# Optimization experiments

Measured on AMD Instinct MI355X. Metric: run time of the kernel, lower is better.

Reference implementation:

```python
import jax, jax.numpy as jnp
import numpy as np

N = 100000
E = 800000
D_IN = 512
D_OUT = 512
EPS = 1e-5


def setup_inputs() -> dict:
    key = jax.random.key(0)
    k = jax.random.split(key, 7)
    x = jax.random.normal(k[0], (N, D_IN), dtype=jnp.float32)
    edge_index = jax.random.randint(k[1], (2, E), 0, N, dtype=jnp.int64)
    # PyG SAGEConv params: lin_l (applied to aggregated neighbors, has bias), lin_r (root weight, no bias)
    W_l = jax.random.normal(k[2], (D_OUT, D_IN), dtype=jnp.float32) * 0.02
    b_l = jnp.zeros((D_OUT,), dtype=jnp.float32)
    W_r = jax.random.normal(k[3], (D_OUT, D_IN), dtype=jnp.float32) * 0.02
    # BatchNorm1d affine params (track_running_stats=False -> always batch stats)
    gamma = jnp.ones((D_OUT,), dtype=jnp.float32)
    beta = jnp.zeros((D_OUT,), dtype=jnp.float32)
    return {"x": x, "edge_index": edge_index, "W_l": W_l, "b_l": b_l,
            "W_r": W_r, "gamma": gamma, "beta": beta}


def reference(x, edge_index, W_l, b_l, W_r, gamma, beta):
    n = x.shape[0]
    src, dst = edge_index[0], edge_index[1]
    # mean-aggregate neighbor features: for each dst node, mean of x[src]
    summed = jax.ops.segment_sum(x[src], dst, num_segments=n)          # [N, D_IN]
    cnt = jax.ops.segment_sum(jnp.ones((src.shape[0],), x.dtype), dst, num_segments=n)
    aggr = summed / jnp.maximum(cnt, 1.0)[:, None]                      # zero-degree -> 0
    # SAGEConv: lin_l(aggr) + lin_r(x)
    h = aggr @ W_l.T + b_l + x @ W_r.T                                  # [N, D_OUT]
    # BatchNorm1d with batch statistics (biased variance), then ReLU
    mu = jnp.mean(h, axis=0)
    var = jnp.mean(jnp.square(h - mu), axis=0)
    h_norm = (h - mu) * jax.lax.rsqrt(var + EPS) * gamma + beta
    return jax.nn.relu(h_norm)
```

## Files before the change

kernel.cpp:

```cpp
#include <hip/hip_runtime.h>
#include <stdint.h>

#define D 512
#define K_TOT 1024
#define EPS 1e-5f
#define CHUNK 1024

typedef __bf16 bf16;
typedef bf16 bf16x8 __attribute__((ext_vector_type(8)));
typedef float f32x4 __attribute__((ext_vector_type(4)));

__global__ void k_convert(const float* __restrict__ x, bf16* __restrict__ xb, size_t total8) {
  size_t i = (size_t)blockIdx.x * blockDim.x + threadIdx.x;
  size_t stride = (size_t)gridDim.x * blockDim.x;
  for (; i < total8; i += stride) {
    float4 a = ((const float4*)x)[i * 2];
    float4 b = ((const float4*)x)[i * 2 + 1];
    bf16x8 v = { (bf16)a.x, (bf16)a.y, (bf16)a.z, (bf16)a.w,
                 (bf16)b.x, (bf16)b.y, (bf16)b.z, (bf16)b.w };
    *(bf16x8*)&xb[i * 8] = v;
  }
}

__global__ void k_degree(const int* __restrict__ dst, int* __restrict__ cnt, int E) {
  int i = blockIdx.x * blockDim.x + threadIdx.x;
  int stride = gridDim.x * blockDim.x;
  for (; i < E; i += stride) atomicAdd(&cnt[dst[i]], 1);
}

__global__ void k_blocksum(const int* __restrict__ cnt, int* __restrict__ bsum, int n) {
  __shared__ int red[4];
  int b = blockIdx.x;
  int base = b * CHUNK;
  int s = 0;
  for (int i = threadIdx.x; i < CHUNK; i += 256) {
    int idx = base + i;
    s += (idx < n) ? cnt[idx] : 0;
  }
#pragma unroll
  for (int o = 32; o > 0; o >>= 1) s += __shfl_down(s, o);
  if ((threadIdx.x & 63) == 0) red[threadIdx.x >> 6] = s;
  __syncthreads();
  if (threadIdx.x == 0) bsum[b] = red[0] + red[1] + red[2] + red[3];
}

__global__ void k_scanb(int* __restrict__ bsum, int* __restrict__ bbase, int nb,
                        int* __restrict__ off, int n, int E) {
  if (threadIdx.x == 0) {
    int run = 0;
    for (int i = 0; i < nb; ++i) { bbase[i] = run; run += bsum[i]; }
    off[n] = E;
  }
}

__global__ void k_offsets(const int* __restrict__ cnt, const int* __restrict__ bbase,
                          int* __restrict__ off, int n) {
  __shared__ int tsum[256];
  int b = blockIdx.x;
  int i0 = b * CHUNK + threadIdx.x * 4;
  int vals[4];
  int s = 0;
#pragma unroll
  for (int j = 0; j < 4; ++j) {
    int idx = i0 + j;
    vals[j] = (idx < n) ? cnt[idx] : 0;
    s += vals[j];
  }
  tsum[threadIdx.x] = s;
  __syncthreads();
  for (int d = 1; d < 256; d <<= 1) {
    int v = (threadIdx.x >= d) ? tsum[threadIdx.x - d] : 0;
    __syncthreads();
    tsum[threadIdx.x] += v;
    __syncthreads();
  }
  int excl = tsum[threadIdx.x] - s + bbase[b];
#pragma unroll
  for (int j = 0; j < 4; ++j) {
    int idx = i0 + j;
    if (idx < n) off[idx] = excl;
    excl += vals[j];
  }
}

__global__ void k_fill(const int* __restrict__ src, const int* __restrict__ dst,
                       const int* __restrict__ off, int* __restrict__ cur,
                       int* __restrict__ csr, int E) {
  int i = blockIdx.x * blockDim.x + threadIdx.x;
  int stride = gridDim.x * blockDim.x;
  for (; i < E; i += stride) {
    int d = dst[i];
    int pos = off[d] + atomicAdd(&cur[d], 1);
    csr[pos] = src[i];
  }
}

__device__ __forceinline__ void acc8(float* c, uint4 u) {
  c[0] += __uint_as_float(u.x << 16);
  c[1] += __uint_as_float(u.x & 0xffff0000u);
  c[2] += __uint_as_float(u.y << 16);
  c[3] += __uint_as_float(u.y & 0xffff0000u);
  c[4] += __uint_as_float(u.z << 16);
  c[5] += __uint_as_float(u.z & 0xffff0000u);
  c[6] += __uint_as_float(u.w << 16);
  c[7] += __uint_as_float(u.w & 0xffff0000u);
}

__global__ __launch_bounds__(256) void k_gather(const bf16* __restrict__ xb,
                                                const int* __restrict__ off,
                                                const int* __restrict__ csr,
                                                bf16* __restrict__ aggr, int n) {
  int node = blockIdx.x * 4 + (threadIdx.x >> 6);
  if (node >= n) return;
  int lane = threadIdx.x & 63;
  int s0 = off[node], s1 = off[node + 1];
  float c[8] = {0.f, 0.f, 0.f, 0.f, 0.f, 0.f, 0.f, 0.f};
  int j = s0;
  for (; j + 3 < s1; j += 4) {
    int i0 = csr[j], i1 = csr[j + 1], i2 = csr[j + 2], i3 = csr[j + 3];
    uint4 u0 = *((const uint4*)(xb + (size_t)i0 * D) + lane);
    uint4 u1 = *((const uint4*)(xb + (size_t)i1 * D) + lane);
    uint4 u2 = *((const uint4*)(xb + (size_t)i2 * D) + lane);
    uint4 u3 = *((const uint4*)(xb + (size_t)i3 * D) + lane);
    acc8(c, u0);
    acc8(c, u1);
    acc8(c, u2);
    acc8(c, u3);
  }
  for (; j < s1; ++j) {
    int a = csr[j];
    uint4 u = *((const uint4*)(xb + (size_t)a * D) + lane);
    acc8(c, u);
  }
  float rinv = (s1 > s0) ? 1.0f / (float)(s1 - s0) : 0.0f;
  bf16x8 out = { (bf16)(c[0] * rinv), (bf16)(c[1] * rinv), (bf16)(c[2] * rinv), (bf16)(c[3] * rinv),
                 (bf16)(c[4] * rinv), (bf16)(c[5] * rinv), (bf16)(c[6] * rinv), (bf16)(c[7] * rinv) };
  *(bf16x8*)&aggr[(size_t)node * D + lane * 8] = out;
}

__global__ void k_build_W(const float* __restrict__ Wl, const float* __restrict__ Wr,
                          bf16* __restrict__ Wc) {
  int i = blockIdx.x * blockDim.x + threadIdx.x;
  if (i >= D * K_TOT) return;
  int o = i >> 10, k = i & 1023;
  float v = (k < D) ? Wr[o * D + k] : Wl[o * D + (k - D)];
  Wc[i] = (bf16)v;
}

__device__ __forceinline__ void gl_lds16(const bf16* g, bf16* l) {
  __builtin_amdgcn_global_load_lds((const __attribute__((address_space(1))) unsigned int*)g,
                                   (__attribute__((address_space(3))) unsigned int*)l, 16, 0, 0);
}

__global__ __launch_bounds__(512, 2) void k_gemm(const bf16* __restrict__ Xb,
                                                 const bf16* __restrict__ Aggr,
                                                 const bf16* __restrict__ Wc,
                                                 const float* __restrict__ bias,
                                                 float* __restrict__ C,
                                                 float* __restrict__ stat, int M) {
  __shared__ __align__(16) bf16 sA0[256 * 64];
  __shared__ __align__(16) bf16 sB0[256 * 64];
  __shared__ __align__(16) bf16 sA1[256 * 64];
  __shared__ __align__(16) bf16 sB1[256 * 64];
  const int tid = threadIdx.x;
  const int lane = tid & 63;
  const int wid = tid >> 6;
  const int wm = wid >> 2;
  const int wn = wid & 3;
  const int fr = lane & 15;
  const int fq = lane >> 4;

  const int bx = blockIdx.x >> 1;
  const int by = blockIdx.x & 1;
  const size_t rowA0 = (size_t)bx * 256;
  const int rowB0 = by * 256;

  const int lrow = tid >> 3;
  const int scol = (((tid & 7) ^ (lrow & 7)) * 8);
  const bf16* pA_x = Xb + (rowA0 + lrow) * D + scol;
  const bf16* pA_g = Aggr + (rowA0 + lrow) * D + scol;
  const bf16* pB = Wc + (size_t)(rowB0 + lrow) * K_TOT + scol;
  bf16* ldsA0 = &sA0[lrow * 64 + (tid & 7) * 8];
  bf16* ldsB0 = &sB0[lrow * 64 + (tid & 7) * 8];
  bf16* ldsA1 = &sA1[lrow * 64 + (tid & 7) * 8];
  bf16* ldsB1 = &sB1[lrow * 64 + (tid & 7) * 8];

  f32x4 acc[8][4] = {};

#define STAGE(t, la, lb) do {                                                   \
    const bf16* As = ((t) < 8) ? pA_x : pA_g;                                   \
    const int ko = ((t) & 7) * 64;                                              \
    _Pragma("unroll")                                                           \
    for (int i = 0; i < 4; ++i) {                                               \
      gl_lds16(As + (size_t)i * 64 * D + ko, (la) + i * 64 * 64);               \
      gl_lds16(pB + (size_t)i * 64 * K_TOT + (t) * 64, (lb) + i * 64 * 64);     \
    }                                                                           \
  } while (0)

#define COMPUTE(sa, sb) do {                                                    \
    _Pragma("unroll")                                                           \
    for (int kk = 0; kk < 2; ++kk) {                                            \
      const int cx = ((kk * 4 + fq) ^ (fr & 7)) * 8;                            \
      bf16x8 aF[8], bF[4];                                                      \
      _Pragma("unroll")                                                         \
      for (int m = 0; m < 8; ++m)                                               \
        aF[m] = *(const bf16x8*)&(sa)[(wm * 128 + m * 16 + fr) * 64 + cx];      \
      _Pragma("unroll")                                                         \
      for (int nn = 0; nn < 4; ++nn)                                            \
        bF[nn] = *(const bf16x8*)&(sb)[(wn * 64 + nn * 16 + fr) * 64 + cx];     \
      _Pragma("unroll")                                                         \
      for (int m = 0; m < 8; ++m)                                               \
        _Pragma("unroll")                                                       \
        for (int nn = 0; nn < 4; ++nn)                                          \
          acc[m][nn] = __builtin_amdgcn_mfma_f32_16x16x32_bf16(aF[m], bF[nn], acc[m][nn], 0, 0, 0); \
    }                                                                           \
  } while (0)

  STAGE(0, ldsA0, ldsB0);
  __syncthreads();
#pragma unroll 1
  for (int t = 0; t < 16; t += 2) {
    STAGE(t + 1, ldsA1, ldsB1);
    COMPUTE(sA0, sB0);
    __syncthreads();
    if (t + 2 < 16) STAGE(t + 2, ldsA0, ldsB0);
    COMPUTE(sA1, sB1);
    __syncthreads();
  }
#undef STAGE
#undef COMPUTE

  const int rowb = (int)rowA0 + wm * 128;
  const int colb = rowB0 + wn * 64;
  float s[4] = {0.f, 0.f, 0.f, 0.f}, q[4] = {0.f, 0.f, 0.f, 0.f};
#pragma unroll
  for (int nn = 0; nn < 4; ++nn) {
    int col = colb + nn * 16 + fr;
    float bv = bias[col];
#pragma unroll
    for (int m = 0; m < 8; ++m) {
      int row0 = rowb + m * 16 + fq * 4;
#pragma unroll
      for (int r = 0; r < 4; ++r) {
        int row = row0 + r;
        if (row < M) {
          float v = acc[m][nn][r] + bv;
          C[(size_t)row * D + col] = v;
          s[nn] += v;
          q[nn] += v * v;
        }
      }
    }
  }
#pragma unroll
  for (int nn = 0; nn < 4; ++nn) {
    float sv = s[nn], qv = q[nn];
    sv += __shfl_down(sv, 32); sv += __shfl_down(sv, 16);
    qv += __shfl_down(qv, 32); qv += __shfl_down(qv, 16);
    if (lane < 16) {
      int col = colb + nn * 16 + fr;
      atomicAdd(&stat[col], sv);
      atomicAdd(&stat[D + col], qv);
    }
  }
}

__global__ void k_finalize(const float* __restrict__ stat, const float* __restrict__ gamma,
                           const float* __restrict__ beta, float* __restrict__ ss, float invn) {
  int c = threadIdx.x;
  float mu = stat[c] * invn;
  float var = stat[D + c] * invn - mu * mu;
  float sc = gamma[c] * rsqrtf(var + EPS);
  ss[c] = sc;
  ss[D + c] = beta[c] - mu * sc;
}

__global__ void k_apply(float* __restrict__ h, const float* __restrict__ ss, int n) {
  size_t i = (size_t)blockIdx.x * blockDim.x + threadIdx.x;
  size_t stride = (size_t)gridDim.x * blockDim.x;
  size_t total = (size_t)n * (D / 4);
  for (; i < total; i += stride) {
    int c4 = ((int)i & 127) * 4;
    float4 v = ((const float4*)h)[i];
    float4 sc = *(const float4*)&ss[c4];
    float4 sh = *(const float4*)&ss[D + c4];
    float4 o;
    o.x = fmaxf(v.x * sc.x + sh.x, 0.f);
    o.y = fmaxf(v.y * sc.y + sh.y, 0.f);
    o.z = fmaxf(v.z * sc.z + sh.z, 0.f);
    o.w = fmaxf(v.w * sc.w + sh.w, 0.f);
    ((float4*)h)[i] = o;
  }
}

extern "C" void kernel_launch(void* const* d_in, const int* in_sizes, int n_in,
                              void* d_out, int out_size, void* d_ws, size_t ws_size,
                              hipStream_t stream) {
  const float* x = (const float*)d_in[0];
  const int* ei = (const int*)d_in[1];
  const float* Wl = (const float*)d_in[2];
  const float* bl = (const float*)d_in[3];
  const float* Wr = (const float*)d_in[4];
  const float* gamma = (const float*)d_in[5];
  const float* beta = (const float*)d_in[6];
  float* out = (float*)d_out;

  const int E = in_sizes[1] / 2;
  const int n = in_sizes[0] / D;
  const int Mpad = ((n + 255) / 256) * 256;
  const int nb = (n + CHUNK - 1) / CHUNK;

  char* ws = (char*)d_ws;
  size_t off_b = 0;
  bf16* Xb   = (bf16*)(ws + off_b); off_b += (size_t)Mpad * D * sizeof(bf16);
  bf16* Aggr = (bf16*)(ws + off_b); off_b += (size_t)Mpad * D * sizeof(bf16);
  bf16* Wc   = (bf16*)(ws + off_b); off_b += (size_t)D * K_TOT * sizeof(bf16);
  int* cnt   = (int*)(ws + off_b);  off_b += (size_t)n * sizeof(int);
  int* offs  = (int*)(ws + off_b);  off_b += (size_t)(n + 1) * sizeof(int);
  int* cur   = (int*)(ws + off_b);  off_b += (size_t)n * sizeof(int);
  int* csr   = (int*)(ws + off_b);  off_b += (size_t)E * sizeof(int);
  int* bsum  = (int*)(ws + off_b);  off_b += 512 * sizeof(int);
  int* bbase = (int*)(ws + off_b);  off_b += 512 * sizeof(int);
  float* stat = (float*)(ws + off_b); off_b += 2 * D * sizeof(float);
  float* ss   = (float*)(ws + off_b);

  const int* srcIdx = ei;
  const int* dstIdx = ei + E;

  hipMemsetAsync(cnt, 0, (size_t)n * sizeof(int), stream);
  hipMemsetAsync(cur, 0, (size_t)n * sizeof(int), stream);
  hipMemsetAsync(stat, 0, 2 * D * sizeof(float), stream);
  hipMemsetAsync(Xb + (size_t)n * D, 0, (size_t)(Mpad - n) * D * sizeof(bf16), stream);
  hipMemsetAsync(Aggr + (size_t)n * D, 0, (size_t)(Mpad - n) * D * sizeof(bf16), stream);

  k_convert<<<2048, 256, 0, stream>>>(x, Xb, (size_t)n * D / 8);
  k_degree<<<1024, 256, 0, stream>>>(dstIdx, cnt, E);
  k_blocksum<<<nb, 256, 0, stream>>>(cnt, bsum, n);
  k_scanb<<<1, 64, 0, stream>>>(bsum, bbase, nb, offs, n, E);
  k_offsets<<<nb, 256, 0, stream>>>(cnt, bbase, offs, n);
  k_fill<<<1024, 256, 0, stream>>>(srcIdx, dstIdx, offs, cur, csr, E);
  k_build_W<<<(D * K_TOT + 255) / 256, 256, 0, stream>>>(Wl, Wr, Wc);
  k_gather<<<(n + 3) / 4, 256, 0, stream>>>(Xb, offs, csr, Aggr, n);
  k_gemm<<<(Mpad / 256) * 2, 512, 0, stream>>>(Xb, Aggr, Wc, bl, out, stat, n);
  k_finalize<<<1, 512, 0, stream>>>(stat, gamma, beta, ss, 1.0f / (float)n);
  k_apply<<<2048, 256, 0, stream>>>(out, ss, n);
}
```

Baseline: 579.8 us.

## Shrink GEMM tile to 128x128, swizzle block order, unroll gather by eight

The GEMM tile shrinks from 256x256 with 512 threads to 128x128 with 256 threads, cutting per-block LDS and accumulator registers so more blocks can be resident at once. Block indices are remapped in chunks of eight, apparently so neighbouring blocks share A and B tiles in cache. The neighbour gather adds an 8-way unrolled loop to keep more loads in flight. Smaller tiles lower arithmetic intensity and raise global traffic for re-reading A and W. The swizzle also assumes the grid size is a multiple of eight.

```diff
diff --git a/kernel.cpp b/kernel.cpp
--- a/kernel.cpp
+++ b/kernel.cpp
@@ -116,16 +116,27 @@
   int s0 = off[node], s1 = off[node + 1];
   float c[8] = {0.f, 0.f, 0.f, 0.f, 0.f, 0.f, 0.f, 0.f};
   int j = s0;
+  for (; j + 7 < s1; j += 8) {
+    int i0 = csr[j], i1 = csr[j + 1], i2 = csr[j + 2], i3 = csr[j + 3];
+    int i4 = csr[j + 4], i5 = csr[j + 5], i6 = csr[j + 6], i7 = csr[j + 7];
+    uint4 u0 = *((const uint4*)(xb + (size_t)i0 * D) + lane);
+    uint4 u1 = *((const uint4*)(xb + (size_t)i1 * D) + lane);
+    uint4 u2 = *((const uint4*)(xb + (size_t)i2 * D) + lane);
+    uint4 u3 = *((const uint4*)(xb + (size_t)i3 * D) + lane);
+    uint4 u4 = *((const uint4*)(xb + (size_t)i4 * D) + lane);
+    uint4 u5 = *((const uint4*)(xb + (size_t)i5 * D) + lane);
+    uint4 u6 = *((const uint4*)(xb + (size_t)i6 * D) + lane);
+    uint4 u7 = *((const uint4*)(xb + (size_t)i7 * D) + lane);
+    acc8(c, u0); acc8(c, u1); acc8(c, u2); acc8(c, u3);
+    acc8(c, u4); acc8(c, u5); acc8(c, u6); acc8(c, u7);
+  }
   for (; j + 3 < s1; j += 4) {
     int i0 = csr[j], i1 = csr[j + 1], i2 = csr[j + 2], i3 = csr[j + 3];
     uint4 u0 = *((const uint4*)(xb + (size_t)i0 * D) + lane);
     uint4 u1 = *((const uint4*)(xb + (size_t)i1 * D) + lane);
     uint4 u2 = *((const uint4*)(xb + (size_t)i2 * D) + lane);
     uint4 u3 = *((const uint4*)(xb + (size_t)i3 * D) + lane);
-    acc8(c, u0);
-    acc8(c, u1);
-    acc8(c, u2);
-    acc8(c, u3);
+    acc8(c, u0); acc8(c, u1); acc8(c, u2); acc8(c, u3);
   }
   for (; j < s1; ++j) {
     int a = csr[j];
@@ -152,28 +163,30 @@
                                    (__attribute__((address_space(3))) unsigned int*)l, 16, 0, 0);
 }
 
-__global__ __launch_bounds__(512, 2) void k_gemm(const bf16* __restrict__ Xb,
+__global__ __launch_bounds__(256, 2) void k_gemm(const bf16* __restrict__ Xb,
                                                  const bf16* __restrict__ Aggr,
                                                  const bf16* __restrict__ Wc,
                                                  const float* __restrict__ bias,
                                                  float* __restrict__ C,
                                                  float* __restrict__ stat, int M) {
-  __shared__ __align__(16) bf16 sA0[256 * 64];
-  __shared__ __align__(16) bf16 sB0[256 * 64];
-  __shared__ __align__(16) bf16 sA1[256 * 64];
-  __shared__ __align__(16) bf16 sB1[256 * 64];
+  __shared__ __align__(16) bf16 sA0[128 * 64];
+  __shared__ __align__(16) bf16 sB0[128 * 64];
+  __shared__ __align__(16) bf16 sA1[128 * 64];
+  __shared__ __align__(16) bf16 sB1[128 * 64];
   const int tid = threadIdx.x;
   const int lane = tid & 63;
   const int wid = tid >> 6;
-  const int wm = wid >> 2;
-  const int wn = wid & 3;
+  const int wm = wid >> 1;
+  const int wn = wid & 1;
   const int fr = lane & 15;
   const int fq = lane >> 4;
 
-  const int bx = blockIdx.x >> 1;
-  const int by = blockIdx.x & 1;
-  const size_t rowA0 = (size_t)bx * 256;
-  const int rowB0 = by * 256;
+  const int cpx = gridDim.x >> 3;
+  const int sw = (blockIdx.x & 7) * cpx + (blockIdx.x >> 3);
+  const int bx = sw >> 2;
+  const int by = sw & 3;
+  const size_t rowA0 = (size_t)bx * 128;
+  const int rowB0 = by * 128;
 
   const int lrow = tid >> 3;
   const int scol = (((tid & 7) ^ (lrow & 7)) * 8);
@@ -185,15 +198,15 @@
   bf16* ldsA1 = &sA1[lrow * 64 + (tid & 7) * 8];
   bf16* ldsB1 = &sB1[lrow * 64 + (tid & 7) * 8];
 
-  f32x4 acc[8][4] = {};
+  f32x4 acc[4][4] = {};
 
 #define STAGE(t, la, lb) do {                                                   \
     const bf16* As = ((t) < 8) ? pA_x : pA_g;                                   \
     const int ko = ((t) & 7) * 64;                                              \
     _Pragma("unroll")                                                           \
-    for (int i = 0; i < 4; ++i) {                                               \
-      gl_lds16(As + (size_t)i * 64 * D + ko, (la) + i * 64 * 64);               \
-      gl_lds16(pB + (size_t)i * 64 * K_TOT + (t) * 64, (lb) + i * 64 * 64);     \
+    for (int j = 0; j < 4; ++j) {                                               \
+      gl_lds16(As + (size_t)j * 32 * D + ko, (la) + j * 32 * 64);               \
+      gl_lds16(pB + (size_t)j * 32 * K_TOT + (t) * 64, (lb) + j * 32 * 64);     \
     }                                                                           \
   } while (0)
 
@@ -201,15 +214,15 @@
     _Pragma("unroll")                                                           \
     for (int kk = 0; kk < 2; ++kk) {                                            \
       const int cx = ((kk * 4 + fq) ^ (fr & 7)) * 8;                            \
-      bf16x8 aF[8], bF[4];                                                      \
+      bf16x8 aF[4], bF[4];                                                      \
       _Pragma("unroll")                                                         \
-      for (int m = 0; m < 8; ++m)                                               \
-        aF[m] = *(const bf16x8*)&(sa)[(wm * 128 + m * 16 + fr) * 64 + cx];      \
+      for (int m = 0; m < 4; ++m)                                               \
+        aF[m] = *(const bf16x8*)&(sa)[(wm * 64 + m * 16 + fr) * 64 + cx];       \
       _Pragma("unroll")                                                         \
       for (int nn = 0; nn < 4; ++nn)                                            \
         bF[nn] = *(const bf16x8*)&(sb)[(wn * 64 + nn * 16 + fr) * 64 + cx];     \
       _Pragma("unroll")                                                         \
-      for (int m = 0; m < 8; ++m)                                               \
+      for (int m = 0; m < 4; ++m)                                               \
         _Pragma("unroll")                                                       \
         for (int nn = 0; nn < 4; ++nn)                                          \
           acc[m][nn] = __builtin_amdgcn_mfma_f32_16x16x32_bf16(aF[m], bF[nn], acc[m][nn], 0, 0, 0); \
@@ -230,7 +243,7 @@
 #undef STAGE
 #undef COMPUTE
 
-  const int rowb = (int)rowA0 + wm * 128;
+  const int rowb = (int)rowA0 + wm * 64;
   const int colb = rowB0 + wn * 64;
   float s[4] = {0.f, 0.f, 0.f, 0.f}, q[4] = {0.f, 0.f, 0.f, 0.f};
 #pragma unroll
@@ -238,7 +251,7 @@
     int col = colb + nn * 16 + fr;
     float bv = bias[col];
 #pragma unroll
-    for (int m = 0; m < 8; ++m) {
+    for (int m = 0; m < 4; ++m) {
       int row0 = rowb + m * 16 + fq * 4;
 #pragma unroll
       for (int r = 0; r < 4; ++r) {
@@ -341,7 +354,7 @@
   k_fill<<<1024, 256, 0, stream>>>(srcIdx, dstIdx, offs, cur, csr, E);
   k_build_W<<<(D * K_TOT + 255) / 256, 256, 0, stream>>>(Wl, Wr, Wc);
   k_gather<<<(n + 3) / 4, 256, 0, stream>>>(Xb, offs, csr, Aggr, n);
-  k_gemm<<<(Mpad / 256) * 2, 512, 0, stream>>>(Xb, Aggr, Wc, bl, out, stat, n);
+  k_gemm<<<(Mpad / 128) * 4, 256, 0, stream>>>(Xb, Aggr, Wc, bl, out, stat, n);
   k_finalize<<<1, 512, 0, stream>>>(stat, gamma, beta, ss, 1.0f / (float)n);
   k_apply<<<2048, 256, 0, stream>>>(out, ss, n);
 }
```

Result: slower. 593.5 us (+2.4%).

## Store GEMM output as bf16 intermediate, fuse memsets and BN finalize into kernels

Applied to the files above, without the earlier changes.

The GEMM epilogue now writes the pre-norm activations as bf16 to a workspace buffer when space allows, and the apply kernel reads that bf16 buffer and writes the fp32 output. This cuts the intermediate write and read traffic roughly in half. The five memsets are folded into the conversion kernel, and the BN finalize kernel is folded into apply, which recomputes scale and shift per element. The gather loop also gets an 8-wide unroll for more loads in flight. The bf16 intermediate adds rounding error before normalization, and the per-element rsqrt adds ALU work.

```diff
diff --git a/kernel.cpp b/kernel.cpp
--- a/kernel.cpp
+++ b/kernel.cpp
@@ -7,11 +7,23 @@
 #define CHUNK 1024
 
 typedef __bf16 bf16;
+typedef bf16 bf16x4 __attribute__((ext_vector_type(4)));
 typedef bf16 bf16x8 __attribute__((ext_vector_type(8)));
 typedef float f32x4 __attribute__((ext_vector_type(4)));
 
-__global__ void k_convert(const float* __restrict__ x, bf16* __restrict__ xb, size_t total8) {
-  size_t i = (size_t)blockIdx.x * blockDim.x + threadIdx.x;
+__global__ void k_prep(const float* __restrict__ x, bf16* __restrict__ xb,
+                       int* __restrict__ cnt, int* __restrict__ cur, float* __restrict__ stat,
+                       bf16* __restrict__ padX, bf16* __restrict__ padA,
+                       int n, int padGroups, size_t total8) {
+  int gid = blockIdx.x * blockDim.x + threadIdx.x;
+  if (gid < n) { cnt[gid] = 0; cur[gid] = 0; }
+  if (gid < 2 * D) stat[gid] = 0.f;
+  if (gid < padGroups) {
+    bf16x8 z = {};
+    *(bf16x8*)&padX[(size_t)gid * 8] = z;
+    *(bf16x8*)&padA[(size_t)gid * 8] = z;
+  }
+  size_t i = (size_t)gid;
   size_t stride = (size_t)gridDim.x * blockDim.x;
   for (; i < total8; i += stride) {
     float4 a = ((const float4*)x)[i * 2];
@@ -116,16 +128,27 @@
   int s0 = off[node], s1 = off[node + 1];
   float c[8] = {0.f, 0.f, 0.f, 0.f, 0.f, 0.f, 0.f, 0.f};
   int j = s0;
+  for (; j + 7 < s1; j += 8) {
+    int i0 = csr[j], i1 = csr[j + 1], i2 = csr[j + 2], i3 = csr[j + 3];
+    int i4 = csr[j + 4], i5 = csr[j + 5], i6 = csr[j + 6], i7 = csr[j + 7];
+    uint4 u0 = *((const uint4*)(xb + (size_t)i0 * D) + lane);
+    uint4 u1 = *((const uint4*)(xb + (size_t)i1 * D) + lane);
+    uint4 u2 = *((const uint4*)(xb + (size_t)i2 * D) + lane);
+    uint4 u3 = *((const uint4*)(xb + (size_t)i3 * D) + lane);
+    uint4 u4 = *((const uint4*)(xb + (size_t)i4 * D) + lane);
+    uint4 u5 = *((const uint4*)(xb + (size_t)i5 * D) + lane);
+    uint4 u6 = *((const uint4*)(xb + (size_t)i6 * D) + lane);
+    uint4 u7 = *((const uint4*)(xb + (size_t)i7 * D) + lane);
+    acc8(c, u0); acc8(c, u1); acc8(c, u2); acc8(c, u3);
+    acc8(c, u4); acc8(c, u5); acc8(c, u6); acc8(c, u7);
+  }
   for (; j + 3 < s1; j += 4) {
     int i0 = csr[j], i1 = csr[j + 1], i2 = csr[j + 2], i3 = csr[j + 3];
     uint4 u0 = *((const uint4*)(xb + (size_t)i0 * D) + lane);
     uint4 u1 = *((const uint4*)(xb + (size_t)i1 * D) + lane);
     uint4 u2 = *((const uint4*)(xb + (size_t)i2 * D) + lane);
     uint4 u3 = *((const uint4*)(xb + (size_t)i3 * D) + lane);
-    acc8(c, u0);
-    acc8(c, u1);
-    acc8(c, u2);
-    acc8(c, u3);
+    acc8(c, u0); acc8(c, u1); acc8(c, u2); acc8(c, u3);
   }
   for (; j < s1; ++j) {
     int a = csr[j];
@@ -152,11 +175,13 @@
                                    (__attribute__((address_space(3))) unsigned int*)l, 16, 0, 0);
 }
 
+template <bool HB>
 __global__ __launch_bounds__(512, 2) void k_gemm(const bf16* __restrict__ Xb,
                                                  const bf16* __restrict__ Aggr,
                                                  const bf16* __restrict__ Wc,
                                                  const float* __restrict__ bias,
-                                                 float* __restrict__ C,
+                                                 bf16* __restrict__ Hb,
+                                                 float* __restrict__ Cf,
                                                  float* __restrict__ stat, int M) {
   __shared__ __align__(16) bf16 sA0[256 * 64];
   __shared__ __align__(16) bf16 sB0[256 * 64];
@@ -245,7 +270,8 @@
         int row = row0 + r;
         if (row < M) {
           float v = acc[m][nn][r] + bv;
-          C[(size_t)row * D + col] = v;
+          if (HB) Hb[(size_t)row * D + col] = (bf16)v;
+          else    Cf[(size_t)row * D + col] = v;
           s[nn] += v;
           q[nn] += v * v;
         }
@@ -265,31 +291,49 @@
   }
 }
 
-__global__ void k_finalize(const float* __restrict__ stat, const float* __restrict__ gamma,
-                           const float* __restrict__ beta, float* __restrict__ ss, float invn) {
-  int c = threadIdx.x;
-  float mu = stat[c] * invn;
-  float var = stat[D + c] * invn - mu * mu;
-  float sc = gamma[c] * rsqrtf(var + EPS);
-  ss[c] = sc;
-  ss[D + c] = beta[c] - mu * sc;
-}
-
-__global__ void k_apply(float* __restrict__ h, const float* __restrict__ ss, int n) {
+template <bool HB>
+__global__ void k_apply(const bf16* __restrict__ hb, const float* __restrict__ hf,
+                        const float* __restrict__ stat, const float* __restrict__ gamma,
+                        const float* __restrict__ beta, float* __restrict__ out,
+                        int n, float invn) {
   size_t i = (size_t)blockIdx.x * blockDim.x + threadIdx.x;
   size_t stride = (size_t)gridDim.x * blockDim.x;
   size_t total = (size_t)n * (D / 4);
   for (; i < total; i += stride) {
     int c4 = ((int)i & 127) * 4;
-    float4 v = ((const float4*)h)[i];
-    float4 sc = *(const float4*)&ss[c4];
-    float4 sh = *(const float4*)&ss[D + c4];
+    float4 v;
+    if (HB) {
+      bf16x4 hv = *(const bf16x4*)&hb[i * 4];
+      v.x = (float)hv[0]; v.y = (float)hv[1]; v.z = (float)hv[2]; v.w = (float)hv[3];
+    } else {
+      v = ((const float4*)hf)[i];
+    }
+    float4 st = *(const float4*)&stat[c4];
+    float4 sq = *(const float4*)&stat[D + c4];
+    float4 gm = *(const float4*)&gamma[c4];
+    float4 bt = *(const float4*)&beta[c4];
     float4 o;
-    o.x = fmaxf(v.x * sc.x + sh.x, 0.f);
-    o.y = fmaxf(v.y * sc.y + sh.y, 0.f);
-    o.z = fmaxf(v.z * sc.z + sh.z, 0.f);
-    o.w = fmaxf(v.w * sc.w + sh.w, 0.f);
-    ((float4*)h)[i] = o;
+    {
+      float mu = st.x * invn, var = sq.x * invn - mu * mu;
+      float sc = gm.x * rsqrtf(var + EPS);
+      o.x = fmaxf(v.x * sc + (bt.x - mu * sc), 0.f);
+    }
+    {
+      float mu = st.y * invn, var = sq.y * invn - mu * mu;
+      float sc = gm.y * rsqrtf(var + EPS);
+      o.y = fmaxf(v.y * sc + (bt.y - mu * sc), 0.f);
+    }
+    {
+      float mu = st.z * invn, var = sq.z * invn - mu * mu;
+      float sc = gm.z * rsqrtf(var + EPS);
+      o.z = fmaxf(v.z * sc + (bt.z - mu * sc), 0.f);
+    }
+    {
+      float mu = st.w * invn, var = sq.w * invn - mu * mu;
+      float sc = gm.w * rsqrtf(var + EPS);
+      o.w = fmaxf(v.w * sc + (bt.w - mu * sc), 0.f);
+    }
+    ((float4*)out)[i] = o;
   }
 }
 
@@ -322,18 +366,18 @@
   int* bsum  = (int*)(ws + off_b);  off_b += 512 * sizeof(int);
   int* bbase = (int*)(ws + off_b);  off_b += 512 * sizeof(int);
   float* stat = (float*)(ws + off_b); off_b += 2 * D * sizeof(float);
-  float* ss   = (float*)(ws + off_b);
+  bf16* Hb   = (bf16*)(ws + off_b);
+  const size_t need_hb = off_b + (size_t)Mpad * D * sizeof(bf16);
+  const bool use_hb = (ws_size >= need_hb);
 
   const int* srcIdx = ei;
   const int* dstIdx = ei + E;
-
-  hipMemsetAsync(cnt, 0, (size_t)n * sizeof(int), stream);
-  hipMemsetAsync(cur, 0, (size_t)n * sizeof(int), stream);
-  hipMemsetAsync(stat, 0, 2 * D * sizeof(float), stream);
-  hipMemsetAsync(Xb + (size_t)n * D, 0, (size_t)(Mpad - n) * D * sizeof(bf16), stream);
-  hipMemsetAsync(Aggr + (size_t)n * D, 0, (size_t)(Mpad - n) * D * sizeof(bf16), stream);
-
-  k_convert<<<2048, 256, 0, stream>>>(x, Xb, (size_t)n * D / 8);
+  const int padGroups = (Mpad - n) * D / 8;
+  const float invn = 1.0f / (float)n;
+
+  k_prep<<<2048, 256, 0, stream>>>(x, Xb, cnt, cur, stat,
+                                   Xb + (size_t)n * D, Aggr + (size_t)n * D,
+                                   n, padGroups, (size_t)n * D / 8);
   k_degree<<<1024, 256, 0, stream>>>(dstIdx, cnt, E);
   k_blocksum<<<nb, 256, 0, stream>>>(cnt, bsum, n);
   k_scanb<<<1, 64, 0, stream>>>(bsum, bbase, nb, offs, n, E);
@@ -341,7 +385,11 @@
   k_fill<<<1024, 256, 0, stream>>>(srcIdx, dstIdx, offs, cur, csr, E);
   k_build_W<<<(D * K_TOT + 255) / 256, 256, 0, stream>>>(Wl, Wr, Wc);
   k_gather<<<(n + 3) / 4, 256, 0, stream>>>(Xb, offs, csr, Aggr, n);
-  k_gemm<<<(Mpad / 256) * 2, 512, 0, stream>>>(Xb, Aggr, Wc, bl, out, stat, n);
-  k_finalize<<<1, 512, 0, stream>>>(stat, gamma, beta, ss, 1.0f / (float)n);
-  k_apply<<<2048, 256, 0, stream>>>(out, ss, n);
-}
+  if (use_hb) {
+    k_gemm<true><<<(Mpad / 256) * 2, 512, 0, stream>>>(Xb, Aggr, Wc, bl, Hb, out, stat, n);
+    k_apply<true><<<2048, 256, 0, stream>>>(Hb, out, stat, gamma, beta, out, n, invn);
+  } else {
+    k_gemm<false><<<(Mpad / 256) * 2, 512, 0, stream>>>(Xb, Aggr, Wc, bl, Hb, out, stat, n);
+    k_apply<false><<<2048, 256, 0, stream>>>(Hb, out, stat, gamma, beta, out, n, invn);
+  }
+}
```

Result: no change. 573.0 us (-1.2%).
